# Optimization experiments

Measured on AMD Instinct MI355X. Metric: run time of the kernel, lower is better.

The kernel has to match this reference:

```python
import jax, jax.numpy as jnp
import numpy as np

FOUR_PI = 4.0 * np.pi
INF_CLAMP = 1e30


def setup_inputs() -> dict:
    key = jax.random.key(0)
    k1, k2, k3, k4 = jax.random.split(key, 4)
    B, N, M, S = 16, 2048, 16, 128
    pcl_transformed = jax.random.normal(k1, (B, N, M, 3), dtype=jnp.float32)
    primitive_points = jax.random.normal(k2, (B, M, S, 3), dtype=jnp.float32)
    size = jax.random.uniform(k3, (B, M, 3), dtype=jnp.float32, minval=0.05, maxval=1.0)
    probs = jax.random.uniform(k4, (B, M), dtype=jnp.float32)
    return {"pcl_transformed": pcl_transformed, "primitive_points": primitive_points,
            "size": size, "probs": probs}


def reference(pcl_transformed, primitive_points, size, probs):
    B, N, M, _ = pcl_transformed.shape
    S = primitive_points.shape[2]

    # diff: (B, M, S, N, 3); dist: (B, M, S, N)
    diff = primitive_points[:, :, :, None, :] - jnp.transpose(pcl_transformed, (0, 2, 1, 3))[:, :, None, :, :]
    dist = jnp.sum(diff * diff, axis=-1)

    # ---- pcl_to_prim loss (min over S, sort over M, stick-breaking cumprod) ----
    d1 = jnp.transpose(jnp.min(dist, axis=2), (0, 2, 1))  # (B, N, M)
    idx = jnp.argsort(d1, axis=-1)                         # (B, N, M)
    distance = jnp.take_along_axis(d1, idx, axis=-1)
    p = jnp.take_along_axis(jnp.broadcast_to(probs[:, None, :], (B, N, M)), idx, axis=-1)
    neg_cumprod = jnp.cumprod(1.0 - p, axis=-1)
    neg_cumprod = jnp.concatenate([jnp.ones_like(neg_cumprod[..., :1]), neg_cumprod[..., :-1]], axis=-1)
    minprob = p * neg_cumprod
    pcl_to_prim = jnp.einsum('bnm,bnm->', distance, minprob) / (B * N)

    # ---- prim_to_pcl loss (min over N, superquadric-area weighting) ----
    d2 = jnp.min(dist, axis=-1)                            # (B, M, S)
    d2 = jnp.where(d2 >= INF_CLAMP, 0.0, d2)
    s0, s1, s2 = size[..., 0], size[..., 1], size[..., 2]
    area = FOUR_PI * ((s0 * s1) ** 1.6 / 3 + (s0 * s2) ** 1.6 / 3 + (s1 * s2) ** 1.6 / 3) ** 0.625
    area = M * area / jnp.sum(area, axis=-1, keepdims=True)  # (B, M)
    prim_to_pcl = jnp.einsum('bm,bm,bm->', jnp.mean(d2, axis=-1), probs, area) / (B * M)

    # No regularizer types enabled -> regs == 0 (matches regularizer_type=[]).
    regs = jnp.zeros((), dtype=pcl_to_prim.dtype)
    total = 1.0 * pcl_to_prim + 1.0 * prim_to_pcl + regs
    return total, pcl_to_prim, prim_to_pcl, regs
```

## Files before the change

### kernel.cpp

```cpp
#include <hip/hip_runtime.h>
#include <math.h>

#define BB 16
#define NN 2048
#define MM 16
#define SS 128

__constant__ const float kFourPi = 12.566370614359172f;

__global__ __launch_bounds__(1024, 4) void fused_dist_kernel(
    const float* __restrict__ pcl,
    const float* __restrict__ prim,
    float* __restrict__ d1,
    float* __restrict__ d2sum,
    unsigned int* __restrict__ counter)
{
    const int bm  = blockIdx.x;
    const int b   = bm >> 4;
    const int m   = bm & 15;
    const int tid = threadIdx.x;

    __shared__ float  Qx[NN], Qy[NN], Qz[NN], Qh[NN];
    __shared__ float4 Plds[SS];
    __shared__ float  d1s[4][NN];
    __shared__ float  wred[16][64];
    __shared__ float  rsum[4];

    if (bm == 0 && tid == 0)
        __hip_atomic_store(counter, 0u, __ATOMIC_RELAXED, __HIP_MEMORY_SCOPE_AGENT);

    {
        const size_t base = ((size_t)(b * NN) * MM + m) * 3;
#pragma unroll
        for (int j = 0; j < 2; ++j) {
            const int n = tid + j * 1024;
            const float* q = pcl + base + (size_t)n * (MM * 3);
            const float x = q[0], y = q[1], z = q[2];
            Qx[n] = x; Qy[n] = y; Qz[n] = z;
            Qh[n] = 0.5f * (x * x + y * y + z * z);
        }
    }
    if (tid < SS) {
        const float* pp = prim + ((size_t)bm * SS + tid) * 3;
        const float x = pp[0], y = pp[1], z = pp[2];
        Plds[tid] = make_float4(x, y, z, 0.5f * (x * x + y * y + z * z));
    }
    __syncthreads();

    const int sub  = tid >> 8;
    const int stid = tid & 255;
    const int s0   = sub * 32;
    const int wid  = tid >> 6;
    const int lane = tid & 63;

    float qx[8], qy[8], qz[8], hq[8], d1m[8];
#pragma unroll
    for (int j = 0; j < 8; ++j) {
        const int n = stid + j * 256;
        qx[j] = Qx[n]; qy[j] = Qy[n]; qz[j] = Qz[n]; hq[j] = Qh[n];
        d1m[j] = 3.0e38f;
    }

    float d2r[32];
#pragma unroll
    for (int s = 0; s < 32; ++s) {
        const float4 f = Plds[s0 + s];
        float e[8];
#pragma unroll
        for (int j = 0; j < 8; ++j) {
            float t = hq[j] + f.w;
            t = fmaf(f.x, -qx[j], t);
            t = fmaf(f.y, -qy[j], t);
            t = fmaf(f.z, -qz[j], t);
            e[j] = t;
            d1m[j] = fminf(d1m[j], t);
        }
        const float m01 = fminf(e[0], e[1]);
        const float m23 = fminf(e[2], e[3]);
        const float m45 = fminf(e[4], e[5]);
        const float m67 = fminf(e[6], e[7]);
        d2r[s] = fminf(fminf(m01, m23), fminf(m45, m67));
    }

#pragma unroll
    for (int j = 0; j < 8; ++j)
        d1s[sub][stid + j * 256] = d1m[j];
    __syncthreads();
#pragma unroll
    for (int j = 0; j < 2; ++j) {
        const int n = tid + j * 1024;
        d1[(size_t)bm * NN + n] = fminf(fminf(d1s[0][n], d1s[1][n]),
                                        fminf(d1s[2][n], d1s[3][n]));
    }

    float v16[16];
    {
        const bool hi = (lane & 32) != 0;
#pragma unroll
        for (int k = 0; k < 16; ++k) {
            const float xk = hi ? d2r[k + 16] : d2r[k];
            const float xs = hi ? d2r[k] : d2r[k + 16];
            v16[k] = fminf(xk, __shfl_xor(xs, 32, 64));
        }
    }
    float v8[8];
    {
        const bool hi = (lane & 16) != 0;
#pragma unroll
        for (int k = 0; k < 8; ++k) {
            const float xk = hi ? v16[k + 8] : v16[k];
            const float xs = hi ? v16[k] : v16[k + 8];
            v8[k] = fminf(xk, __shfl_xor(xs, 16, 64));
        }
    }
    float v4[4];
    {
        const bool hi = (lane & 8) != 0;
#pragma unroll
        for (int k = 0; k < 4; ++k) {
            const float xk = hi ? v8[k + 4] : v8[k];
            const float xs = hi ? v8[k] : v8[k + 4];
            v4[k] = fminf(xk, __shfl_xor(xs, 8, 64));
        }
    }
    float v2a, v2b;
    {
        const bool hi = (lane & 4) != 0;
        const float xk0 = hi ? v4[2] : v4[0];
        const float xs0 = hi ? v4[0] : v4[2];
        v2a = fminf(xk0, __shfl_xor(xs0, 4, 64));
        const float xk1 = hi ? v4[3] : v4[1];
        const float xs1 = hi ? v4[1] : v4[3];
        v2b = fminf(xk1, __shfl_xor(xs1, 4, 64));
    }
    float v1;
    {
        const bool hi = (lane & 2) != 0;
        const float xk = hi ? v2b : v2a;
        const float xs = hi ? v2a : v2b;
        v1 = fminf(xk, __shfl_xor(xs, 2, 64));
    }
    const float r = fminf(v1, __shfl_xor(v1, 1, 64));
    wred[wid][lane] = r;
    __syncthreads();

    if (tid < 256) {
        const int sc = tid >> 6;
        const int l  = tid & 63;
        float mv = fminf(fminf(wred[sc * 4 + 0][l], wred[sc * 4 + 1][l]),
                         fminf(wred[sc * 4 + 2][l], wred[sc * 4 + 3][l]));
        if (mv >= 5.0e29f) mv = 0.0f;
#pragma unroll
        for (int off = 32; off > 0; off >>= 1)
            mv += __shfl_down(mv, off, 64);
        if (l == 0) rsum[sc] = mv;
    }
    __syncthreads();
    if (tid == 0) d2sum[bm] = rsum[0] + rsum[1] + rsum[2] + rsum[3];
}

__global__ __launch_bounds__(256) void p2p_final_kernel(
    const float* __restrict__ d1,
    const float* __restrict__ probs,
    const float* __restrict__ size_,
    const float* __restrict__ d2sum,
    float* __restrict__ partial,
    unsigned int* __restrict__ counter,
    float* __restrict__ out)
{
    const int tid = threadIdx.x;
    const int gid = blockIdx.x * 256 + tid;
    const int b   = gid >> 11;
    const int n   = gid & (NN - 1);

    float d[16], p[16];
#pragma unroll
    for (int m = 0; m < 16; ++m) {
        const float mn = d1[((size_t)(b * MM + m)) * NN + n];
        d[m] = mn + mn;
    }

    const float* pb = probs + b * MM;
#pragma unroll
    for (int k = 0; k < 16; ++k) p[k] = pb[k];

#define CE(i, j)                                              \
    {                                                         \
        const bool c = d[i] > d[j];                           \
        const float td = c ? d[j] : d[i];                     \
        d[j] = c ? d[i] : d[j];  d[i] = td;                   \
        const float tp = c ? p[j] : p[i];                     \
        p[j] = c ? p[i] : p[j];  p[i] = tp;                   \
    }
#pragma unroll
    for (int r = 0; r < 16; ++r) {
        if ((r & 1) == 0) {
            CE(0, 1) CE(2, 3) CE(4, 5) CE(6, 7)
            CE(8, 9) CE(10, 11) CE(12, 13) CE(14, 15)
        } else {
            CE(1, 2) CE(3, 4) CE(5, 6) CE(7, 8)
            CE(9, 10) CE(11, 12) CE(13, 14)
        }
    }
#undef CE

    float acc = 1.0f, sum = 0.0f;
#pragma unroll
    for (int k = 0; k < 16; ++k) {
        sum += d[k] * p[k] * acc;
        acc *= (1.0f - p[k]);
    }

    const int wid  = tid >> 6;
    const int lane = tid & 63;
    __shared__ float red4[4];
#pragma unroll
    for (int off = 32; off > 0; off >>= 1)
        sum += __shfl_down(sum, off, 64);
    if (lane == 0) red4[wid] = sum;
    __syncthreads();

    __shared__ bool amLast;
    if (tid == 0) {
        const float bsum = red4[0] + red4[1] + red4[2] + red4[3];
        __hip_atomic_store(&partial[blockIdx.x], bsum,
                           __ATOMIC_RELEASE, __HIP_MEMORY_SCOPE_AGENT);
        const unsigned int prev = __hip_atomic_fetch_add(
            counter, 1u, __ATOMIC_ACQ_REL, __HIP_MEMORY_SCOPE_AGENT);
        amLast = (prev == 127u);
    }
    __syncthreads();
    if (!amLast) return;

    const int fb = tid >> 4;

    __shared__ float  areaSh[256];
    __shared__ double redA[4];
    __shared__ double redB[4];

    const float s0 = size_[tid * 3 + 0];
    const float s1 = size_[tid * 3 + 1];
    const float s2 = size_[tid * 3 + 2];
    const float inner = powf(s0 * s1, 1.6f) * (1.0f / 3.0f)
                      + powf(s0 * s2, 1.6f) * (1.0f / 3.0f)
                      + powf(s1 * s2, 1.6f) * (1.0f / 3.0f);
    const float a = kFourPi * powf(inner, 0.625f);
    areaSh[tid] = a;
    __syncthreads();

    float asum = 0.0f;
#pragma unroll
    for (int mm = 0; mm < 16; ++mm) asum += areaSh[fb * 16 + mm];
    const float anorm = 16.0f * a / asum;

    double t = (double)(d2sum[tid] * (1.0f / 128.0f)) * (double)probs[tid] * (double)anorm;
#pragma unroll
    for (int off = 32; off > 0; off >>= 1)
        t += __shfl_down(t, off, 64);
    if (lane == 0) redA[wid] = t;

    double u = 0.0;
    if (tid < 128) {
        const float pv = __hip_atomic_load(&partial[tid],
                                           __ATOMIC_ACQUIRE, __HIP_MEMORY_SCOPE_AGENT);
        u = (double)pv;
    }
#pragma unroll
    for (int off = 32; off > 0; off >>= 1)
        u += __shfl_down(u, off, 64);
    if (lane == 0) redB[wid] = u;

    __syncthreads();
    if (tid == 0) {
        const double prim_to_pcl = (redA[0] + redA[1] + redA[2] + redA[3]) / 256.0;
        const double pcl_to_prim = (redB[0] + redB[1] + redB[2] + redB[3]) / 32768.0;
        out[0] = (float)(pcl_to_prim + prim_to_pcl);
        out[1] = (float)pcl_to_prim;
        out[2] = (float)prim_to_pcl;
        out[3] = 0.0f;
    }
}


extern "C" void kernel_launch(void* const* d_in, const int* in_sizes, int n_in,
                              void* d_out, int out_size, void* d_ws, size_t ws_size,
                              hipStream_t stream) {
    const float* pcl   = (const float*)d_in[0];
    const float* prim  = (const float*)d_in[1];
    const float* size_ = (const float*)d_in[2];
    const float* probs = (const float*)d_in[3];
    float* out = (float*)d_out;

    float* d1             = (float*)d_ws;
    float* d2sum          = d1 + (size_t)256 * NN;
    float* partial        = d2sum + 256;
    unsigned int* counter = (unsigned int*)(partial + 128);

    fused_dist_kernel<<<BB * MM, 1024, 0, stream>>>(pcl, prim, d1, d2sum, counter);
    p2p_final_kernel<<<128, 256, 0, stream>>>(d1, probs, size_, d2sum, partial, counter, out);
}
```

Before: 89.48 us.

## Split distance kernel into N-chunks and reduce prim-to-pcl minima via global atomicMin

Replaces the one-block-per-(b,m) distance kernel, which staged data in LDS with 1024 threads, by a 4-chunk grid of 256-thread blocks. Each block holds two points per thread in registers and reads primitive points straight from global memory. Per-sample minima over N are combined across chunks and waves with unsigned atomicMin into a buffer pre-filled by an extra memset, and the final kernel then sums 128 entries per (b,m). This removes LDS staging and block barriers and spreads the work over more blocks. In exchange it adds an extra memset launch, many global atomics and repeated shuffle reductions.

```diff
diff --git a/kernel.cpp b/kernel.cpp
--- a/kernel.cpp
+++ b/kernel.cpp
@@ -8,162 +8,119 @@
 
 __constant__ const float kFourPi = 12.566370614359172f;
 
-__global__ __launch_bounds__(1024, 4) void fused_dist_kernel(
+__global__ __launch_bounds__(256, 4) void dist_kernel(
     const float* __restrict__ pcl,
     const float* __restrict__ prim,
     float* __restrict__ d1,
-    float* __restrict__ d2sum,
+    unsigned int* __restrict__ d2min,
     unsigned int* __restrict__ counter)
 {
-    const int bm  = blockIdx.x;
-    const int b   = bm >> 4;
-    const int m   = bm & 15;
-    const int tid = threadIdx.x;
-
-    __shared__ float  Qx[NN], Qy[NN], Qz[NN], Qh[NN];
-    __shared__ float4 Plds[SS];
-    __shared__ float  d1s[4][NN];
-    __shared__ float  wred[16][64];
-    __shared__ float  rsum[4];
-
-    if (bm == 0 && tid == 0)
+    const int bm    = blockIdx.x;
+    const int chunk = blockIdx.y;
+    const int b     = bm >> 4;
+    const int m     = bm & 15;
+    const int tid   = threadIdx.x;
+    const int lane  = tid & 63;
+
+    if (bm == 0 && chunk == 0 && tid == 0)
         __hip_atomic_store(counter, 0u, __ATOMIC_RELAXED, __HIP_MEMORY_SCOPE_AGENT);
 
-    {
-        const size_t base = ((size_t)(b * NN) * MM + m) * 3;
-#pragma unroll
-        for (int j = 0; j < 2; ++j) {
-            const int n = tid + j * 1024;
-            const float* q = pcl + base + (size_t)n * (MM * 3);
-            const float x = q[0], y = q[1], z = q[2];
-            Qx[n] = x; Qy[n] = y; Qz[n] = z;
-            Qh[n] = 0.5f * (x * x + y * y + z * z);
-        }
-    }
-    if (tid < SS) {
-        const float* pp = prim + ((size_t)bm * SS + tid) * 3;
-        const float x = pp[0], y = pp[1], z = pp[2];
-        Plds[tid] = make_float4(x, y, z, 0.5f * (x * x + y * y + z * z));
-    }
-    __syncthreads();
-
-    const int sub  = tid >> 8;
-    const int stid = tid & 255;
-    const int s0   = sub * 32;
-    const int wid  = tid >> 6;
-    const int lane = tid & 63;
-
-    float qx[8], qy[8], qz[8], hq[8], d1m[8];
-#pragma unroll
-    for (int j = 0; j < 8; ++j) {
-        const int n = stid + j * 256;
-        qx[j] = Qx[n]; qy[j] = Qy[n]; qz[j] = Qz[n]; hq[j] = Qh[n];
-        d1m[j] = 3.0e38f;
-    }
-
-    float d2r[32];
-#pragma unroll
-    for (int s = 0; s < 32; ++s) {
-        const float4 f = Plds[s0 + s];
-        float e[8];
-#pragma unroll
-        for (int j = 0; j < 8; ++j) {
-            float t = hq[j] + f.w;
-            t = fmaf(f.x, -qx[j], t);
-            t = fmaf(f.y, -qy[j], t);
-            t = fmaf(f.z, -qz[j], t);
-            e[j] = t;
-            d1m[j] = fminf(d1m[j], t);
-        }
-        const float m01 = fminf(e[0], e[1]);
-        const float m23 = fminf(e[2], e[3]);
-        const float m45 = fminf(e[4], e[5]);
-        const float m67 = fminf(e[6], e[7]);
-        d2r[s] = fminf(fminf(m01, m23), fminf(m45, m67));
-    }
-
-#pragma unroll
-    for (int j = 0; j < 8; ++j)
-        d1s[sub][stid + j * 256] = d1m[j];
-    __syncthreads();
-#pragma unroll
-    for (int j = 0; j < 2; ++j) {
-        const int n = tid + j * 1024;
-        d1[(size_t)bm * NN + n] = fminf(fminf(d1s[0][n], d1s[1][n]),
-                                        fminf(d1s[2][n], d1s[3][n]));
-    }
-
-    float v16[16];
-    {
-        const bool hi = (lane & 32) != 0;
-#pragma unroll
-        for (int k = 0; k < 16; ++k) {
-            const float xk = hi ? d2r[k + 16] : d2r[k];
-            const float xs = hi ? d2r[k] : d2r[k + 16];
-            v16[k] = fminf(xk, __shfl_xor(xs, 32, 64));
-        }
-    }
-    float v8[8];
-    {
-        const bool hi = (lane & 16) != 0;
-#pragma unroll
-        for (int k = 0; k < 8; ++k) {
-            const float xk = hi ? v16[k + 8] : v16[k];
-            const float xs = hi ? v16[k] : v16[k + 8];
-            v8[k] = fminf(xk, __shfl_xor(xs, 16, 64));
-        }
-    }
-    float v4[4];
-    {
-        const bool hi = (lane & 8) != 0;
-#pragma unroll
-        for (int k = 0; k < 4; ++k) {
-            const float xk = hi ? v8[k + 4] : v8[k];
-            const float xs = hi ? v8[k] : v8[k + 4];
-            v4[k] = fminf(xk, __shfl_xor(xs, 8, 64));
-        }
-    }
-    float v2a, v2b;
-    {
-        const bool hi = (lane & 4) != 0;
-        const float xk0 = hi ? v4[2] : v4[0];
-        const float xs0 = hi ? v4[0] : v4[2];
-        v2a = fminf(xk0, __shfl_xor(xs0, 4, 64));
-        const float xk1 = hi ? v4[3] : v4[1];
-        const float xs1 = hi ? v4[1] : v4[3];
-        v2b = fminf(xk1, __shfl_xor(xs1, 4, 64));
-    }
-    float v1;
-    {
-        const bool hi = (lane & 2) != 0;
-        const float xk = hi ? v2b : v2a;
-        const float xs = hi ? v2a : v2b;
-        v1 = fminf(xk, __shfl_xor(xs, 2, 64));
-    }
-    const float r = fminf(v1, __shfl_xor(v1, 1, 64));
-    wred[wid][lane] = r;
-    __syncthreads();
-
-    if (tid < 256) {
-        const int sc = tid >> 6;
-        const int l  = tid & 63;
-        float mv = fminf(fminf(wred[sc * 4 + 0][l], wred[sc * 4 + 1][l]),
-                         fminf(wred[sc * 4 + 2][l], wred[sc * 4 + 3][l]));
-        if (mv >= 5.0e29f) mv = 0.0f;
-#pragma unroll
-        for (int off = 32; off > 0; off >>= 1)
-            mv += __shfl_down(mv, off, 64);
-        if (l == 0) rsum[sc] = mv;
-    }
-    __syncthreads();
-    if (tid == 0) d2sum[bm] = rsum[0] + rsum[1] + rsum[2] + rsum[3];
+    const int n0 = chunk * 512;
+    const float* q0p = pcl + ((size_t)(b * NN + n0 + tid) * MM + m) * 3;
+    const float* q1p = q0p + (size_t)256 * MM * 3;
+    const float q0x = q0p[0], q0y = q0p[1], q0z = q0p[2];
+    const float q1x = q1p[0], q1y = q1p[1], q1z = q1p[2];
+    const float hq0 = 0.5f * (q0x * q0x + q0y * q0y + q0z * q0z);
+    const float hq1 = 0.5f * (q1x * q1x + q1y * q1y + q1z * q1z);
+
+    float d1m0 = 3.0e38f, d1m1 = 3.0e38f;
+
+#pragma unroll
+    for (int g = 0; g < 4; ++g) {
+        const float* pr = prim + (size_t)(bm * SS + g * 32) * 3;
+        float d2r[32];
+#pragma unroll
+        for (int s = 0; s < 32; ++s) {
+            const float px = pr[3 * s + 0];
+            const float py = pr[3 * s + 1];
+            const float pz = pr[3 * s + 2];
+            const float hs = 0.5f * fmaf(pz, pz, fmaf(py, py, px * px));
+            float e0 = hq0 + hs;
+            e0 = fmaf(px, -q0x, e0);
+            e0 = fmaf(py, -q0y, e0);
+            e0 = fmaf(pz, -q0z, e0);
+            float e1 = hq1 + hs;
+            e1 = fmaf(px, -q1x, e1);
+            e1 = fmaf(py, -q1y, e1);
+            e1 = fmaf(pz, -q1z, e1);
+            d1m0 = fminf(d1m0, e0);
+            d1m1 = fminf(d1m1, e1);
+            d2r[s] = fminf(e0, e1);
+        }
+
+        float v16[16];
+        {
+            const bool hi = (lane & 32) != 0;
+#pragma unroll
+            for (int k = 0; k < 16; ++k) {
+                const float xk = hi ? d2r[k + 16] : d2r[k];
+                const float xs = hi ? d2r[k] : d2r[k + 16];
+                v16[k] = fminf(xk, __shfl_xor(xs, 32, 64));
+            }
+        }
+        float v8[8];
+        {
+            const bool hi = (lane & 16) != 0;
+#pragma unroll
+            for (int k = 0; k < 8; ++k) {
+                const float xk = hi ? v16[k + 8] : v16[k];
+                const float xs = hi ? v16[k] : v16[k + 8];
+                v8[k] = fminf(xk, __shfl_xor(xs, 16, 64));
+            }
+        }
+        float v4[4];
+        {
+            const bool hi = (lane & 8) != 0;
+#pragma unroll
+            for (int k = 0; k < 4; ++k) {
+                const float xk = hi ? v8[k + 4] : v8[k];
+                const float xs = hi ? v8[k] : v8[k + 4];
+                v4[k] = fminf(xk, __shfl_xor(xs, 8, 64));
+            }
+        }
+        float v2a, v2b;
+        {
+            const bool hi = (lane & 4) != 0;
+            const float xk0 = hi ? v4[2] : v4[0];
+            const float xs0 = hi ? v4[0] : v4[2];
+            v2a = fminf(xk0, __shfl_xor(xs0, 4, 64));
+            const float xk1 = hi ? v4[3] : v4[1];
+            const float xs1 = hi ? v4[1] : v4[3];
+            v2b = fminf(xk1, __shfl_xor(xs1, 4, 64));
+        }
+        float v1;
+        {
+            const bool hi = (lane & 2) != 0;
+            const float xk = hi ? v2b : v2a;
+            const float xs = hi ? v2a : v2b;
+            v1 = fminf(xk, __shfl_xor(xs, 2, 64));
+        }
+        float r = fminf(v1, __shfl_xor(v1, 1, 64));
+        r = fmaxf(r, 0.0f);
+        if ((lane & 1) == 0)
+            atomicMin(&d2min[(unsigned)(g * 32 + (lane >> 1)) * 256 + bm],
+                      __float_as_uint(r));
+    }
+
+    d1[(size_t)bm * NN + n0 + tid]       = d1m0;
+    d1[(size_t)bm * NN + n0 + tid + 256] = d1m1;
 }
 
 __global__ __launch_bounds__(256) void p2p_final_kernel(
     const float* __restrict__ d1,
     const float* __restrict__ probs,
     const float* __restrict__ size_,
-    const float* __restrict__ d2sum,
+    const unsigned int* __restrict__ d2min,
     float* __restrict__ partial,
     unsigned int* __restrict__ counter,
     float* __restrict__ out)
@@ -253,7 +210,14 @@
     for (int mm = 0; mm < 16; ++mm) asum += areaSh[fb * 16 + mm];
     const float anorm = 16.0f * a / asum;
 
-    double t = (double)(d2sum[tid] * (1.0f / 128.0f)) * (double)probs[tid] * (double)anorm;
+    float dsum = 0.0f;
+#pragma unroll 8
+    for (int k = 0; k < 128; ++k) {
+        float v = __uint_as_float(d2min[(unsigned)k * 256 + tid]);
+        if (v >= 5.0e29f) v = 0.0f;
+        dsum += v;
+    }
+    double t = (double)(dsum * (1.0f / 64.0f)) * (double)probs[tid] * (double)anorm;
 #pragma unroll
     for (int off = 32; off > 0; off >>= 1)
         t += __shfl_down(t, off, 64);
@@ -291,11 +255,13 @@
     const float* probs = (const float*)d_in[3];
     float* out = (float*)d_out;
 
-    float* d1             = (float*)d_ws;
-    float* d2sum          = d1 + (size_t)256 * NN;
-    float* partial        = d2sum + 256;
+    float*        d1      = (float*)d_ws;
+    unsigned int* d2min   = (unsigned int*)(d1 + (size_t)256 * NN);
+    float*        partial = (float*)(d2min + 128 * 256);
     unsigned int* counter = (unsigned int*)(partial + 128);
 
-    fused_dist_kernel<<<BB * MM, 1024, 0, stream>>>(pcl, prim, d1, d2sum, counter);
-    p2p_final_kernel<<<128, 256, 0, stream>>>(d1, probs, size_, d2sum, partial, counter, out);
+    hipMemsetAsync(d2min, 0x7f, (size_t)128 * 256 * sizeof(unsigned int), stream);
+
+    dist_kernel<<<dim3(BB * MM, 4), 256, 0, stream>>>(pcl, prim, d1, d2min, counter);
+    p2p_final_kernel<<<128, 256, 0, stream>>>(d1, probs, size_, d2min, partial, counter, out);
 }
```

Measured after the change: 148.0 us. 1.65x slower.
